# Kernel tuning notes

Hardware: AMD Instinct MI355X
Metric: run time of the kernel (lower is better)

Reference implementation:

```python
import jax, jax.numpy as jnp
import numpy as np

B, S, D = 8, 2048, 1024
EXPERTS = 8
CAPACITY = 512  # moe_expert_capacity, per batch row along seq axis


def setup_inputs() -> dict:
    key = jax.random.key(0)
    k1, k2, k3 = jax.random.split(key, 3)
    norm_data = jax.random.normal(k1, (B, S, D), dtype=jnp.float32)
    gate_w = jax.random.normal(k2, (EXPERTS, D), dtype=jnp.float32) * 0.02   # nn.Linear weight [E, d]
    expert_w = jax.random.normal(k3, (EXPERTS, D, D), dtype=jnp.float32) * 0.02  # per-expert dense (expert_fn)
    return {"norm_data": norm_data, "gate_w": gate_w, "expert_w": expert_w}


def reference(norm_data, gate_w, expert_w):
    # --- route ---
    router_logits = jnp.einsum('bsd,ed->bse', norm_data, gate_w)            # [B,S,E]
    router_probs = jax.nn.softmax(router_logits.astype(jnp.float32), axis=-1)
    top_expert = jnp.argmax(router_probs, axis=-1)                           # [B,S]
    onehot = jax.nn.one_hot(top_expert, EXPERTS, dtype=jnp.int32)            # [B,S,E]
    token_priority = jnp.cumsum(onehot, axis=-2)                             # cumsum over seq dim
    router_mask = onehot * (token_priority <= CAPACITY).astype(jnp.int32)    # drop over-capacity tokens
    top_prob = jnp.max(router_probs, axis=-1, keepdims=True)                 # [B,S,1]

    # --- dispatch / expert / combine (dropped tokens pass through identity) ---
    next_states = norm_data
    for e in range(EXPERTS):
        out_e = jnp.einsum('bsd,df->bsf', norm_data, expert_w[e])            # [B,S,D]
        keep = (router_mask[:, :, e] > 0)[..., None]                         # [B,S,1]
        next_states = jnp.where(keep, out_e.astype(norm_data.dtype), next_states)

    hidden_states = top_prob.astype(norm_data.dtype) * next_states
    expert_index = jnp.argmax(router_mask, axis=-1)                          # [B,S]
    return (hidden_states, router_logits, expert_index)
```

## Files before the change

### kernel.cpp

```cpp
#include <hip/hip_runtime.h>
#include <hip/hip_bf16.h>
#include <stdint.h>


typedef __attribute__((ext_vector_type(8))) short short8;
typedef __attribute__((ext_vector_type(4))) float f32x4;

#define AS1 __attribute__((address_space(1)))
#define AS3 __attribute__((address_space(3)))

static __device__ __forceinline__ uint32_t f2bf(float f) {
  __hip_bfloat16 h = __float2bfloat16(f);
  return (uint32_t)*reinterpret_cast<unsigned short*>(&h);
}

__global__ __launch_bounds__(256) void k_router(
    const float* __restrict__ x, const float* __restrict__ gw,
    __hip_bfloat16* __restrict__ xb, float* __restrict__ logits,
    float* __restrict__ tprob, int* __restrict__ texp) {
  __shared__ __align__(16) float gs[8 * 1024];
  const int tid = threadIdx.x;
  {
    const float4* g4 = reinterpret_cast<const float4*>(gw);
    float4* s4 = reinterpret_cast<float4*>(gs);
#pragma unroll
    for (int i = 0; i < 8; ++i) s4[tid + 256 * i] = g4[tid + 256 * i];
  }
  __syncthreads();
  const int wave = tid >> 6, lane = tid & 63;
  const int t = blockIdx.x * 4 + wave;
  const float2* x2 = reinterpret_cast<const float2*>(x + (size_t)t * 1024);
  uint32_t* xbu = reinterpret_cast<uint32_t*>(xb + (size_t)t * 1024);
  const float2* g2 = reinterpret_cast<const float2*>(gs);
  float acc[8];
#pragma unroll
  for (int e = 0; e < 8; ++e) acc[e] = 0.f;
#pragma unroll
  for (int kk = 0; kk < 8; ++kk) {
    int p = lane + 64 * kk;
    float2 xv = x2[p];
    xbu[p] = f2bf(xv.x) | (f2bf(xv.y) << 16);
#pragma unroll
    for (int e = 0; e < 8; ++e) {
      float2 g = g2[e * 512 + p];
      acc[e] = fmaf(xv.x, g.x, acc[e]);
      acc[e] = fmaf(xv.y, g.y, acc[e]);
    }
  }
#pragma unroll
  for (int d = 1; d < 64; d <<= 1) {
#pragma unroll
    for (int e = 0; e < 8; ++e) acc[e] += __shfl_xor(acc[e], d, 64);
  }
  if (lane == 0) {
    float m = acc[0];
    int idx = 0;
#pragma unroll
    for (int e = 1; e < 8; ++e)
      if (acc[e] > m) { m = acc[e]; idx = e; }
    float s = 0.f;
#pragma unroll
    for (int e = 0; e < 8; ++e) s += expf(acc[e] - m);
    tprob[t] = 1.0f / s;
    texp[t] = idx;
#pragma unroll
    for (int e = 0; e < 8; ++e) logits[(size_t)t * 8 + e] = acc[e];
  }
}

__global__ __launch_bounds__(256) void k_wconv(const float* __restrict__ w,
                                               __hip_bfloat16* __restrict__ wt) {
  const int bx = blockIdx.x;
  const int e = bx >> 10;
  const int rem = bx & 1023;
  const int k0 = (rem >> 5) << 5;
  const int n0 = (rem & 31) << 5;
  __shared__ float tile[32][33];
  const int tid = threadIdx.x;
  const int c = tid & 31, r0 = tid >> 5;
  const float* ws = w + (size_t)e * 1024 * 1024;
#pragma unroll
  for (int i = 0; i < 4; ++i) {
    int r = r0 + 8 * i;
    tile[r][c] = ws[(size_t)(k0 + r) * 1024 + n0 + c];
  }
  __syncthreads();
  __hip_bfloat16* wd = wt + (size_t)e * 1024 * 1024;
#pragma unroll
  for (int i = 0; i < 4; ++i) {
    int r = r0 + 8 * i;
    wd[(size_t)(n0 + r) * 1024 + k0 + c] = __float2bfloat16(tile[c][r]);
  }
}

__global__ __launch_bounds__(256) void k_scan(
    const int* __restrict__ texp, int* __restrict__ slots, int* __restrict__ neb,
    int* __restrict__ keep, float* __restrict__ idx_out) {
  const int b = blockIdx.x;
  const int tid = threadIdx.x;
  __shared__ int te_s[2048];
#pragma unroll
  for (int i = 0; i < 8; ++i) te_s[tid + 256 * i] = texp[b * 2048 + tid + 256 * i];
  __syncthreads();

  int myte[8], cnt[8];
#pragma unroll
  for (int e = 0; e < 8; ++e) cnt[e] = 0;
#pragma unroll
  for (int j = 0; j < 8; ++j) {
    int v = te_s[tid * 8 + j];
    myte[j] = v;
#pragma unroll
    for (int e = 0; e < 8; ++e) cnt[e] += (v == e);
  }
  unsigned u0 = (unsigned)cnt[0] | ((unsigned)cnt[1] << 16);
  unsigned u1 = (unsigned)cnt[2] | ((unsigned)cnt[3] << 16);
  unsigned u2 = (unsigned)cnt[4] | ((unsigned)cnt[5] << 16);
  unsigned u3 = (unsigned)cnt[6] | ((unsigned)cnt[7] << 16);
  const int lane = tid & 63, wave = tid >> 6;
#pragma unroll
  for (int d = 1; d < 64; d <<= 1) {
    unsigned v0 = __shfl_up(u0, d, 64);
    unsigned v1 = __shfl_up(u1, d, 64);
    unsigned v2 = __shfl_up(u2, d, 64);
    unsigned v3 = __shfl_up(u3, d, 64);
    if (lane >= d) { u0 += v0; u1 += v1; u2 += v2; u3 += v3; }
  }
  __shared__ unsigned wtot[4][4];
  if (lane == 63) { wtot[wave][0] = u0; wtot[wave][1] = u1; wtot[wave][2] = u2; wtot[wave][3] = u3; }
  __syncthreads();
  unsigned a0 = 0, a1 = 0, a2 = 0, a3 = 0, s0 = 0, s1 = 0, s2 = 0, s3 = 0;
#pragma unroll
  for (int w = 0; w < 4; ++w) {
    unsigned q0 = wtot[w][0], q1 = wtot[w][1], q2 = wtot[w][2], q3 = wtot[w][3];
    if (w < wave) { a0 += q0; a1 += q1; a2 += q2; a3 += q3; }
    s0 += q0; s1 += q1; s2 += q2; s3 += q3;
  }
  u0 += a0; u1 += a1; u2 += a2; u3 += a3;
  int base[8];
  base[0] = (int)(u0 & 0xFFFF) - cnt[0]; base[1] = (int)(u0 >> 16) - cnt[1];
  base[2] = (int)(u1 & 0xFFFF) - cnt[2]; base[3] = (int)(u1 >> 16) - cnt[3];
  base[4] = (int)(u2 & 0xFFFF) - cnt[4]; base[5] = (int)(u2 >> 16) - cnt[5];
  base[6] = (int)(u3 & 0xFFFF) - cnt[6]; base[7] = (int)(u3 >> 16) - cnt[7];
  if (tid == 0) {
    int tt[8] = {(int)(s0 & 0xFFFF), (int)(s0 >> 16), (int)(s1 & 0xFFFF), (int)(s1 >> 16),
                 (int)(s2 & 0xFFFF), (int)(s2 >> 16), (int)(s3 & 0xFFFF), (int)(s3 >> 16)};
#pragma unroll
    for (int e = 0; e < 8; ++e) neb[e * 8 + b] = tt[e] < 512 ? tt[e] : 512;
  }
#pragma unroll
  for (int j = 0; j < 8; ++j) {
    int v = myte[j];
    int rank = 0;
#pragma unroll
    for (int e = 0; e < 8; ++e)
      if (v == e) { base[e] += 1; rank = base[e]; }
    int tok = b * 2048 + tid * 8 + j;
    int kp = rank <= 512;
    keep[tok] = kp;
    idx_out[tok] = kp ? (float)v : 0.0f;
    if (kp) slots[v * 4096 + b * 512 + rank - 1] = tok;
  }
}

__global__ __launch_bounds__(256) void k_compact(
    const int* __restrict__ neb, const int* __restrict__ slots,
    int* __restrict__ comp, int* __restrict__ tot) {
  const int e = blockIdx.x;
  const int tid = threadIdx.x;
  __shared__ int ofs[8];
  if (tid == 0) {
    int s = 0;
#pragma unroll
    for (int b = 0; b < 8; ++b) { ofs[b] = s; s += neb[e * 8 + b]; }
    tot[e] = s;
  }
  __syncthreads();
#pragma unroll
  for (int b = 0; b < 8; ++b) {
    int c = neb[e * 8 + b];
    int o = ofs[b];
    for (int i = tid; i < c; i += 256)
      comp[e * 4096 + o + i] = slots[e * 4096 + b * 512 + i];
  }
}

__global__ __launch_bounds__(256, 3) void k_gemm(
    const __hip_bfloat16* __restrict__ xb, const __hip_bfloat16* __restrict__ wt,
    const int* __restrict__ comp, const int* __restrict__ tot,
    const float* __restrict__ tprob, float* __restrict__ out) {
  int pf[9];
  pf[0] = 0;
#pragma unroll
  for (int e = 0; e < 8; ++e) pf[e + 1] = pf[e] + ((tot[e] + 127) >> 7) * 8;
  const int T = pf[8];
  const int bid = blockIdx.x;
  if (bid >= T) return;
  const int q8 = T >> 3, r8 = T & 7, xcd = bid & 7, pos = bid >> 3;
  const int tile = (xcd < r8 ? xcd * (q8 + 1) : r8 * (q8 + 1) + (xcd - r8) * q8) + pos;
  int e = 0;
#pragma unroll
  for (int k = 0; k < 8; ++k)
    if (tile >= pf[k + 1]) e = k + 1;
  const int local = tile - pf[e];
  const int rt = local >> 3;
  const int ct = local & 7;
  int nvalid = tot[e] - rt * 128;
  if (nvalid > 128) nvalid = 128;

  __shared__ __align__(16) __hip_bfloat16 sm[3][2][128 * 32];
  __shared__ int rid_s[128];
  __shared__ float tp_s[128];

  const int tid = threadIdx.x;
  const int* seg = comp + e * 4096 + rt * 128;
  if (tid < 128) {
    int rid = seg[(tid < nvalid) ? tid : 0];
    rid_s[tid] = rid;
    tp_s[tid] = tprob[rid];
  }
  __syncthreads();

  const int wave = tid >> 6, lane = tid & 63;
  const int wm = wave >> 1, wn = wave & 1;

  const __hip_bfloat16* wte = wt + (size_t)e * 1024 * 1024;
  const __hip_bfloat16* pa[2];
  const __hip_bfloat16* pb[2];
#pragma unroll
  for (int p = 0; p < 2; ++p) {
    int cid = p * 256 + tid;
    int row = cid >> 2, slot = cid & 3;
    int kl = slot ^ ((row >> 1) & 3);
    pa[p] = xb + (size_t)rid_s[row] * 1024 + kl * 8;
    pb[p] = wte + (size_t)(ct * 128 + row) * 1024 + kl * 8;
  }

#define STAGE(kti, bufi)                                                           \
  do {                                                                             \
    _Pragma("unroll") for (int p = 0; p < 2; ++p) {                                \
      __builtin_amdgcn_global_load_lds((const AS1 uint32_t*)(pa[p] + (kti) * 32),  \
                                       (AS3 uint32_t*)&sm[bufi][0][(p * 256 + tid) * 8], 16, 0, 0); \
      __builtin_amdgcn_global_load_lds((const AS1 uint32_t*)(pb[p] + (kti) * 32),  \
                                       (AS3 uint32_t*)&sm[bufi][1][(p * 256 + tid) * 8], 16, 0, 0); \
    }                                                                              \
  } while (0)

  f32x4 acc[4][4];
#pragma unroll
  for (int i = 0; i < 4; ++i)
#pragma unroll
    for (int j = 0; j < 4; ++j) acc[i][j] = 0.f;

  const int frow = lane & 15;
  const int qq = lane >> 4;
  const int sl = qq ^ ((frow >> 1) & 3);
  const int aoff = (wm * 64 + frow) * 32 + sl * 8;
  const int boff = (wn * 64 + frow) * 32 + sl * 8;

  STAGE(0, 0);
  STAGE(1, 1);

#define COMPUTE(bufi)                                                              \
  do {                                                                             \
    const __hip_bfloat16* As = &sm[bufi][0][0];                                    \
    const __hip_bfloat16* Bs = &sm[bufi][1][0];                                    \
    short8 a[4], b[4];                                                             \
    _Pragma("unroll") for (int mi = 0; mi < 4; ++mi)                               \
        a[mi] = *reinterpret_cast<const short8*>(&As[aoff + mi * 512]);            \
    _Pragma("unroll") for (int ni = 0; ni < 4; ++ni)                               \
        b[ni] = *reinterpret_cast<const short8*>(&Bs[boff + ni * 512]);            \
    asm volatile("s_waitcnt lgkmcnt(0)" ::: "memory");                             \
    __builtin_amdgcn_sched_barrier(0);                                             \
    __builtin_amdgcn_s_setprio(1);                                                 \
    _Pragma("unroll") for (int mi = 0; mi < 4; ++mi)                               \
        _Pragma("unroll") for (int ni = 0; ni < 4; ++ni)                           \
            acc[mi][ni] = __builtin_amdgcn_mfma_f32_16x16x32_bf16(a[mi], b[ni], acc[mi][ni], 0, 0, 0); \
    __builtin_amdgcn_s_setprio(0);                                                 \
  } while (0)

  for (int t = 0; t < 31; ++t) {
    asm volatile("s_waitcnt vmcnt(4)" ::: "memory");
    __builtin_amdgcn_s_barrier();
    if (t + 2 < 32) STAGE(t + 2, (t + 2) % 3);
    COMPUTE(t % 3);
  }
  asm volatile("s_waitcnt vmcnt(0)" ::: "memory");
  __builtin_amdgcn_s_barrier();
  COMPUTE(31 % 3);
#undef COMPUTE
#undef STAGE

  const int colb = ct * 128 + wn * 64 + frow;
  const int rowb = wm * 64 + qq * 4;
#pragma unroll
  for (int mi = 0; mi < 4; ++mi) {
#pragma unroll
    for (int j = 0; j < 4; ++j) {
      int r = rowb + mi * 16 + j;
      if (r < nvalid) {
        size_t ro = (size_t)rid_s[r] * 1024;
        float sc = tp_s[r];
#pragma unroll
        for (int ni = 0; ni < 4; ++ni)
          out[ro + colb + ni * 16] = sc * acc[mi][ni][j];
      }
    }
  }
}

__global__ __launch_bounds__(256) void k_identity(
    const float* __restrict__ x, const float* __restrict__ tprob,
    const int* __restrict__ keep, float* __restrict__ out) {
  const int t0 = blockIdx.x * 8;
  const int tid = threadIdx.x;
#pragma unroll
  for (int j = 0; j < 8; ++j) {
    int t = t0 + j;
    if (!keep[t]) {
      float s = tprob[t];
      const float4* xi = reinterpret_cast<const float4*>(x + (size_t)t * 1024);
      float4* o = reinterpret_cast<float4*>(out + (size_t)t * 1024);
      float4 v = xi[tid];
      o[tid] = make_float4(s * v.x, s * v.y, s * v.z, s * v.w);
    }
  }
}

extern "C" void kernel_launch(void* const* d_in, const int* in_sizes, int n_in,
                              void* d_out, int out_size, void* d_ws, size_t ws_size,
                              hipStream_t stream) {
  const float* x = (const float*)d_in[0];
  const float* gw = (const float*)d_in[1];
  const float* w = (const float*)d_in[2];
  float* out = (float*)d_out;
  float* logits = out + (size_t)16384 * 1024;
  float* idx_out = logits + (size_t)16384 * 8;

  char* ws = (char*)d_ws;
  __hip_bfloat16* xb = (__hip_bfloat16*)(ws);
  __hip_bfloat16* wt = (__hip_bfloat16*)(ws + 33554432);
  float* tprob = (float*)(ws + 50331648);
  int* texp   = (int*)(ws + 50397184);
  int* keep   = (int*)(ws + 50462720);
  int* slots  = (int*)(ws + 50528256);
  int* neb    = (int*)(ws + 50659328);
  int* comp   = (int*)(ws + 50659584);
  int* tot    = (int*)(ws + 50790656);

  hipLaunchKernelGGL(k_router,   dim3(4096), dim3(256), 0, stream, x, gw, xb, logits, tprob, texp);
  hipLaunchKernelGGL(k_wconv,    dim3(8192), dim3(256), 0, stream, w, wt);
  hipLaunchKernelGGL(k_scan,     dim3(8),    dim3(256), 0, stream, texp, slots, neb, keep, idx_out);
  hipLaunchKernelGGL(k_compact,  dim3(8),    dim3(256), 0, stream, neb, slots, comp, tot);
  hipLaunchKernelGGL(k_gemm,     dim3(1088), dim3(256), 0, stream, xb, wt, comp, tot, tprob, out);
  hipLaunchKernelGGL(k_identity, dim3(2048), dim3(256), 0, stream, x, tprob, keep, out);
}
```

Measured before the change: 111.1 us.

## Enlarge expert GEMM tiles to 256x256 with 512-thread blocks and BK=64

Reworks the per-expert grouped GEMM from 128x128 tiles with 256 threads and a three-stage BK=32 pipeline into 256x256 tiles with 512 threads. It now uses a two-stage BK=64 pipeline held in 128KB of dynamic LDS with an 8-way XOR swizzle. Each wave computes a 128x64 sub-tile, which raises arithmetic intensity and cuts redundant global and L2 loads of activations and weights. The cost is far fewer tiles, so many CUs may sit idle. It also adds a barrier before each refill and relies on a large dynamic LDS allocation.

```diff
diff --git a/kernel.cpp b/kernel.cpp
--- a/kernel.cpp
+++ b/kernel.cpp
@@ -185,14 +185,14 @@
   }
 }
 
-__global__ __launch_bounds__(256, 3) void k_gemm(
+__global__ __launch_bounds__(512, 2) void k_gemm(
     const __hip_bfloat16* __restrict__ xb, const __hip_bfloat16* __restrict__ wt,
     const int* __restrict__ comp, const int* __restrict__ tot,
     const float* __restrict__ tprob, float* __restrict__ out) {
   int pf[9];
   pf[0] = 0;
 #pragma unroll
-  for (int e = 0; e < 8; ++e) pf[e + 1] = pf[e] + ((tot[e] + 127) >> 7) * 8;
+  for (int e = 0; e < 8; ++e) pf[e + 1] = pf[e] + ((tot[e] + 255) >> 8) * 4;
   const int T = pf[8];
   const int bid = blockIdx.x;
   if (bid >= T) return;
@@ -203,18 +203,18 @@
   for (int k = 0; k < 8; ++k)
     if (tile >= pf[k + 1]) e = k + 1;
   const int local = tile - pf[e];
-  const int rt = local >> 3;
-  const int ct = local & 7;
-  int nvalid = tot[e] - rt * 128;
-  if (nvalid > 128) nvalid = 128;
-
-  __shared__ __align__(16) __hip_bfloat16 sm[3][2][128 * 32];
-  __shared__ int rid_s[128];
-  __shared__ float tp_s[128];
-
-  const int tid = threadIdx.x;
-  const int* seg = comp + e * 4096 + rt * 128;
-  if (tid < 128) {
+  const int rt = local >> 2;
+  const int ct = local & 3;
+  int nvalid = tot[e] - rt * 256;
+  if (nvalid > 256) nvalid = 256;
+
+  extern __shared__ __align__(16) char dynls[];
+  __shared__ int rid_s[256];
+  __shared__ float tp_s[256];
+
+  const int tid = threadIdx.x;
+  const int* seg = comp + e * 4096 + rt * 256;
+  if (tid < 256) {
     int rid = seg[(tid < nvalid) ? tid : 0];
     rid_s[tid] = rid;
     tp_s[tid] = tprob[rid];
@@ -222,79 +222,88 @@
   __syncthreads();
 
   const int wave = tid >> 6, lane = tid & 63;
-  const int wm = wave >> 1, wn = wave & 1;
+  const int wm = wave >> 2, wn = wave & 3;
 
   const __hip_bfloat16* wte = wt + (size_t)e * 1024 * 1024;
-  const __hip_bfloat16* pa[2];
-  const __hip_bfloat16* pb[2];
-#pragma unroll
-  for (int p = 0; p < 2; ++p) {
-    int cid = p * 256 + tid;
-    int row = cid >> 2, slot = cid & 3;
-    int kl = slot ^ ((row >> 1) & 3);
+  const __hip_bfloat16* pa[4];
+  const __hip_bfloat16* pb[4];
+#pragma unroll
+  for (int p = 0; p < 4; ++p) {
+    int cid = p * 512 + tid;
+    int row = cid >> 3, slot = cid & 7;
+    int kl = slot ^ (row & 7);
     pa[p] = xb + (size_t)rid_s[row] * 1024 + kl * 8;
-    pb[p] = wte + (size_t)(ct * 128 + row) * 1024 + kl * 8;
-  }
-
-#define STAGE(kti, bufi)                                                           \
-  do {                                                                             \
-    _Pragma("unroll") for (int p = 0; p < 2; ++p) {                                \
-      __builtin_amdgcn_global_load_lds((const AS1 uint32_t*)(pa[p] + (kti) * 32),  \
-                                       (AS3 uint32_t*)&sm[bufi][0][(p * 256 + tid) * 8], 16, 0, 0); \
-      __builtin_amdgcn_global_load_lds((const AS1 uint32_t*)(pb[p] + (kti) * 32),  \
-                                       (AS3 uint32_t*)&sm[bufi][1][(p * 256 + tid) * 8], 16, 0, 0); \
-    }                                                                              \
+    pb[p] = wte + (size_t)(ct * 256 + row) * 1024 + kl * 8;
+  }
+
+#define STAGE(kti, bufi)                                                            \
+  do {                                                                              \
+    char* db_ = dynls + (bufi) * 65536;                                             \
+    _Pragma("unroll") for (int p = 0; p < 4; ++p) {                                 \
+      __builtin_amdgcn_global_load_lds((const AS1 uint32_t*)(pa[p] + (kti) * 64),   \
+                                       (AS3 uint32_t*)(db_ + (p * 512 + tid) * 16), 16, 0, 0); \
+      __builtin_amdgcn_global_load_lds((const AS1 uint32_t*)(pb[p] + (kti) * 64),   \
+                                       (AS3 uint32_t*)(db_ + 32768 + (p * 512 + tid) * 16), 16, 0, 0); \
+    }                                                                               \
   } while (0)
 
-  f32x4 acc[4][4];
-#pragma unroll
-  for (int i = 0; i < 4; ++i)
+  f32x4 acc[8][4];
+#pragma unroll
+  for (int i = 0; i < 8; ++i)
 #pragma unroll
     for (int j = 0; j < 4; ++j) acc[i][j] = 0.f;
 
   const int frow = lane & 15;
   const int qq = lane >> 4;
-  const int sl = qq ^ ((frow >> 1) & 3);
-  const int aoff = (wm * 64 + frow) * 32 + sl * 8;
-  const int boff = (wn * 64 + frow) * 32 + sl * 8;
+  const int sw = frow & 7;
+  const int abase = (wm * 128 + frow) * 64;
+  const int bbase = (wn * 64 + frow) * 64;
+  const int sl0 = (qq) ^ sw;
+  const int sl1 = (4 + qq) ^ sw;
+
+#define COMPUTE(bufi)                                                               \
+  do {                                                                              \
+    const __hip_bfloat16* As = (const __hip_bfloat16*)(dynls + (bufi) * 65536);     \
+    const __hip_bfloat16* Bs = As + 16384;                                          \
+    _Pragma("unroll") for (int ks = 0; ks < 2; ++ks) {                              \
+      const int slk = ks ? sl1 : sl0;                                               \
+      short8 a[8], b[4];                                                            \
+      _Pragma("unroll") for (int mi = 0; mi < 8; ++mi)                              \
+          a[mi] = *reinterpret_cast<const short8*>(&As[abase + mi * 1024 + slk * 8]); \
+      _Pragma("unroll") for (int ni = 0; ni < 4; ++ni)                              \
+          b[ni] = *reinterpret_cast<const short8*>(&Bs[bbase + ni * 1024 + slk * 8]); \
+      asm volatile("s_waitcnt lgkmcnt(0)" ::: "memory");                            \
+      __builtin_amdgcn_sched_barrier(0);                                            \
+      __builtin_amdgcn_s_setprio(1);                                                \
+      _Pragma("unroll") for (int mi = 0; mi < 8; ++mi)                              \
+          _Pragma("unroll") for (int ni = 0; ni < 4; ++ni)                          \
+              acc[mi][ni] = __builtin_amdgcn_mfma_f32_16x16x32_bf16(a[mi], b[ni], acc[mi][ni], 0, 0, 0); \
+      __builtin_amdgcn_s_setprio(0);                                                \
+    }                                                                               \
+  } while (0)
 
   STAGE(0, 0);
   STAGE(1, 1);
-
-#define COMPUTE(bufi)                                                              \
-  do {                                                                             \
-    const __hip_bfloat16* As = &sm[bufi][0][0];                                    \
-    const __hip_bfloat16* Bs = &sm[bufi][1][0];                                    \
-    short8 a[4], b[4];                                                             \
-    _Pragma("unroll") for (int mi = 0; mi < 4; ++mi)                               \
-        a[mi] = *reinterpret_cast<const short8*>(&As[aoff + mi * 512]);            \
-    _Pragma("unroll") for (int ni = 0; ni < 4; ++ni)                               \
-        b[ni] = *reinterpret_cast<const short8*>(&Bs[boff + ni * 512]);            \
-    asm volatile("s_waitcnt lgkmcnt(0)" ::: "memory");                             \
-    __builtin_amdgcn_sched_barrier(0);                                             \
-    __builtin_amdgcn_s_setprio(1);                                                 \
-    _Pragma("unroll") for (int mi = 0; mi < 4; ++mi)                               \
-        _Pragma("unroll") for (int ni = 0; ni < 4; ++ni)                           \
-            acc[mi][ni] = __builtin_amdgcn_mfma_f32_16x16x32_bf16(a[mi], b[ni], acc[mi][ni], 0, 0, 0); \
-    __builtin_amdgcn_s_setprio(0);                                                 \
-  } while (0)
-
-  for (int t = 0; t < 31; ++t) {
-    asm volatile("s_waitcnt vmcnt(4)" ::: "memory");
+  for (int t = 0; t < 16; ++t) {
+    if (t < 15) {
+      asm volatile("s_waitcnt vmcnt(8)" ::: "memory");
+    } else {
+      asm volatile("s_waitcnt vmcnt(0)" ::: "memory");
+    }
     __builtin_amdgcn_s_barrier();
-    if (t + 2 < 32) STAGE(t + 2, (t + 2) % 3);
-    COMPUTE(t % 3);
-  }
-  asm volatile("s_waitcnt vmcnt(0)" ::: "memory");
-  __builtin_amdgcn_s_barrier();
-  COMPUTE(31 % 3);
+    __builtin_amdgcn_sched_barrier(0);
+    COMPUTE(t & 1);
+    __builtin_amdgcn_s_barrier();
+    __builtin_amdgcn_sched_barrier(0);
+    if (t + 2 < 16) STAGE(t + 2, t & 1);
+  }
 #undef COMPUTE
 #undef STAGE
 
-  const int colb = ct * 128 + wn * 64 + frow;
-  const int rowb = wm * 64 + qq * 4;
-#pragma unroll
-  for (int mi = 0; mi < 4; ++mi) {
+  const int colb = ct * 256 + wn * 64 + frow;
+  const int rowb = wm * 128 + qq * 4;
+#pragma unroll
+  for (int mi = 0; mi < 8; ++mi) {
 #pragma unroll
     for (int j = 0; j < 4; ++j) {
       int r = rowb + mi * 16 + j;
@@ -352,6 +361,6 @@
   hipLaunchKernelGGL(k_wconv,    dim3(8192), dim3(256), 0, stream, w, wt);
   hipLaunchKernelGGL(k_scan,     dim3(8),    dim3(256), 0, stream, texp, slots, neb, keep, idx_out);
   hipLaunchKernelGGL(k_compact,  dim3(8),    dim3(256), 0, stream, neb, slots, comp, tot);
-  hipLaunchKernelGGL(k_gemm,     dim3(1088), dim3(256), 0, stream, xb, wt, comp, tot, tprob, out);
+  hipLaunchKernelGGL(k_gemm,     dim3(512),  dim3(512), 131072, stream, xb, wt, comp, tot, tprob, out);
   hipLaunchKernelGGL(k_identity, dim3(2048), dim3(256), 0, stream, x, tprob, keep, out);
 }
```

New measurement: 121.2 us. 9.1% more time.
